# Kernel tuning notes

Hardware: AMD Instinct MI355X
Metric: run time of the kernel (lower is better)

The kernel has to match this reference:

```python
import jax, jax.numpy as jnp
import numpy as np

# Static 4-level feature pyramid (H, W) per level; total tokens = 20197
SHAPES = [(100, 152), (50, 76), (25, 38), (13, 19)]
B, S, E, H, L, P, R = 4, 1024, 256, 8, 4, 20, 4
HD = E // H
OFFSET_SCALE = 4.0


def setup_inputs() -> dict:
    key = jax.random.key(0)
    ks = jax.random.split(key, 11)
    total = sum(h * w for h, w in SHAPES)
    s = 0.02
    return {
        "x": jax.random.normal(ks[0], (B, S, E), jnp.float32),
        "encoder_input": jax.random.normal(ks[1], (B, total, E), jnp.float32),
        "v_w": jax.random.normal(ks[2], (E, E), jnp.float32) * s,
        "out_w": jax.random.normal(ks[3], (E, E), jnp.float32) * s,
        "off_w": jax.random.normal(ks[4], (H * L * P * 2, E), jnp.float32) * s,
        "off_b": jax.random.normal(ks[5], (H * L * P * 2,), jnp.float32) * s,
        "attn_w": jax.random.normal(ks[6], (H * L * P, E), jnp.float32) * s,
        "attn_b": jax.random.normal(ks[7], (H * L * P,), jnp.float32) * s,
        "ref_w": jax.random.normal(ks[8], (H * R, E), jnp.float32) * s,
        "ref_b": jax.random.normal(ks[9], (H * R,), jnp.float32) * s,
        "def_refs": jax.random.uniform(ks[10], (R, 2), jnp.float32, 0.1, 0.9),
        "spatial_shapes": jnp.array(SHAPES, dtype=jnp.int32),
    }


def _grid_sample(img, gx, gy, Hh, Ww):
    """Bilinear grid_sample, padding_mode='zeros', align_corners=False.
    img: (N, C, Hh*Ww); gx, gy: (N, M) in [-1, 1]. Returns (N, C, M)."""
    x = ((gx + 1.0) * Ww - 1.0) * 0.5
    y = ((gy + 1.0) * Hh - 1.0) * 0.5
    x0 = jnp.floor(x)
    y0 = jnp.floor(y)
    wx = x - x0
    wy = y - y0
    x0i = x0.astype(jnp.int32)
    y0i = y0.astype(jnp.int32)
    N, C, _ = img.shape

    def gather(xi, yi):
        valid = (xi >= 0) & (xi < Ww) & (yi >= 0) & (yi < Hh)
        idx = jnp.clip(yi, 0, Hh - 1) * Ww + jnp.clip(xi, 0, Ww - 1)
        v = jnp.take_along_axis(
            img, jnp.broadcast_to(idx[:, None, :], (N, C, idx.shape[-1])), axis=2)
        return v * valid[:, None, :].astype(img.dtype)

    return (gather(x0i, y0i) * ((1 - wx) * (1 - wy))[:, None, :]
            + gather(x0i + 1, y0i) * (wx * (1 - wy))[:, None, :]
            + gather(x0i, y0i + 1) * ((1 - wx) * wy)[:, None, :]
            + gather(x0i + 1, y0i + 1) * (wx * wy)[:, None, :])


def reference(x, encoder_input, v_w, out_w, off_w, off_b, attn_w, attn_b,
              ref_w, ref_b, def_refs, spatial_shapes):
    b, s, _ = x.shape
    values = (encoder_input @ v_w.T).reshape(b, -1, H, HD)
    refs = jax.nn.sigmoid(def_refs)  # (R, 2), default reference points
    ref_mix = jax.nn.softmax((x @ ref_w.T + ref_b).reshape(b, s, H, R), axis=-1)
    anchors = jnp.einsum('bshr,rc->bshc', ref_mix, refs)  # (b, s, H, 2)
    offsets = (x @ off_w.T + off_b).reshape(b, s, H, L, P, 2)
    attn = jax.nn.softmax((x @ attn_w.T + attn_b).reshape(b, s, H, L * P),
                          axis=-1).reshape(b, s, H, L, P)

    out = jnp.zeros((b, s, H, HD), x.dtype)
    start = 0
    for lvl, (hh, ww) in enumerate(SHAPES):  # static per-level loop (L=4)
        img = values[:, start:start + hh * ww]  # (b, hh*ww, H, HD)
        start += hh * ww
        img = img.transpose(0, 2, 3, 1).reshape(b * H, HD, hh * ww)
        norm = jnp.array([max(ww, 1), max(hh, 1)], x.dtype)
        locs = anchors[:, :, :, None, :] + jnp.tanh(offsets[:, :, :, lvl]) * (OFFSET_SCALE / norm)
        grid = jnp.clip(locs, 0.0, 1.0) * 2.0 - 1.0  # (b, s, H, P, 2)
        grid = grid.transpose(0, 2, 1, 3, 4).reshape(b * H, s * P, 2)
        sampled = _grid_sample(img, grid[..., 0], grid[..., 1], hh, ww)  # (b*H, HD, s*P)
        sampled = sampled.reshape(b, H, HD, s, P)
        out = out + jnp.einsum('bhcsp,bshp->bshc', sampled, attn[:, :, :, lvl])
    return out.reshape(b, s, E) @ out_w.T
```

## Files before the change

kernel.cpp:

```cpp
#include <hip/hip_runtime.h>
#include <hip/hip_bf16.h>
#include <math.h>

#define NH 8
#define HD 32
#define EDIM 256
#define NL 4
#define NP 20
#define NR 4
#define SEQ 1024
#define BATCH 4
#define TOTAL 20197
#define OFF_SCALE 4.0f

#define M_ENC (BATCH * TOTAL)
#define KDIM 256
#define LDSW 40

typedef short bf16x8 __attribute__((ext_vector_type(8)));
typedef float f32x4  __attribute__((ext_vector_type(4)));

__device__ __forceinline__ unsigned short f32_to_bf16_rne(float f) {
    unsigned u = __float_as_uint(f);
    return (unsigned short)((u + 0x7fffu + ((u >> 16) & 1u)) >> 16);
}

__global__ __launch_bounds__(256) void cast_f32_bf16_kernel(
    const float* __restrict__ src, unsigned short* __restrict__ dst,
    long n)
{
    long i = (long)blockIdx.x * blockDim.x + threadIdx.x;
    long stride = (long)gridDim.x * blockDim.x;
    for (long e = i * 8; e < n; e += stride * 8) {
        float4 a = *reinterpret_cast<const float4*>(src + e);
        float4 b = *reinterpret_cast<const float4*>(src + e + 4);
        float f[8] = {a.x, a.y, a.z, a.w, b.x, b.y, b.z, b.w};
        unsigned short o[8];
        #pragma unroll
        for (int j = 0; j < 8; ++j) o[j] = f32_to_bf16_rne(f[j]);
        *reinterpret_cast<uint4*>(dst + e) = *reinterpret_cast<const uint4*>(o);
    }
}

__global__ __launch_bounds__(256) void gemm_mfma_f32a_kernel(
    const float* __restrict__ A,
    const unsigned short* __restrict__ W,
    const float* __restrict__ bias,
    float* __restrict__ C,
    int M_real, int N)
{
    __shared__ __align__(16) unsigned short As[128 * LDSW];
    __shared__ __align__(16) unsigned short Ws[128 * LDSW];

    const int tid  = threadIdx.x;
    const int m0   = blockIdx.x * 128;
    const int n0   = blockIdx.y * 128;
    const int wave = tid >> 6;
    const int lane = tid & 63;
    const int wr   = wave >> 1;
    const int wc   = wave & 1;
    const int lrow = lane & 15;
    const int kg   = lane >> 4;

    f32x4 acc[4][4] = {};

    for (int k0 = 0; k0 < KDIM; k0 += 32) {
        #pragma unroll
        for (int p = 0; p < 4; ++p) {
            int s   = tid + p * 256;
            int row = s >> 3;
            int sl  = s & 7;
            int gm  = m0 + row;
            float4 v = make_float4(0.f, 0.f, 0.f, 0.f);
            if (gm < M_real)
                v = *reinterpret_cast<const float4*>(&A[(size_t)gm * KDIM + k0 + sl * 4]);
            unsigned short o[4] = {
                f32_to_bf16_rne(v.x), f32_to_bf16_rne(v.y),
                f32_to_bf16_rne(v.z), f32_to_bf16_rne(v.w)};
            *reinterpret_cast<uint2*>(&As[row * LDSW + sl * 4]) =
                *reinterpret_cast<const uint2*>(o);
        }
        #pragma unroll
        for (int it = 0; it < 2; ++it) {
            int s   = tid + it * 256;
            int row = s >> 2;
            int ks  = s & 3;
            uint4 vw = *reinterpret_cast<const uint4*>(
                W + (size_t)(n0 + row) * KDIM + k0 + ks * 8);
            *reinterpret_cast<uint4*>(&Ws[row * LDSW + ks * 8]) = vw;
        }
        __syncthreads();

        bf16x8 af[4], bfr[4];
        #pragma unroll
        for (int mi = 0; mi < 4; ++mi)
            af[mi] = *reinterpret_cast<const bf16x8*>(
                &As[(wr * 64 + mi * 16 + lrow) * LDSW + kg * 8]);
        #pragma unroll
        for (int nj = 0; nj < 4; ++nj)
            bfr[nj] = *reinterpret_cast<const bf16x8*>(
                &Ws[(wc * 64 + nj * 16 + lrow) * LDSW + kg * 8]);
        #pragma unroll
        for (int mi = 0; mi < 4; ++mi)
            #pragma unroll
            for (int nj = 0; nj < 4; ++nj)
                acc[mi][nj] = __builtin_amdgcn_mfma_f32_16x16x32_bf16(
                    af[mi], bfr[nj], acc[mi][nj], 0, 0, 0);
        __syncthreads();
    }

    #pragma unroll
    for (int mi = 0; mi < 4; ++mi) {
        #pragma unroll
        for (int nj = 0; nj < 4; ++nj) {
            int row_base = m0 + wr * 64 + mi * 16 + kg * 4;
            int col      = n0 + wc * 64 + nj * 16 + lrow;
            float bv = bias ? bias[col] : 0.f;
            #pragma unroll
            for (int r = 0; r < 4; ++r) {
                int row = row_base + r;
                if (row < M_real)
                    C[(size_t)row * N + col] = acc[mi][nj][r] + bv;
            }
        }
    }
}

__global__ __launch_bounds__(256) void gemm_atb_kernel(
    const float* __restrict__ A, const float* __restrict__ W,
    const float* __restrict__ bias, float* __restrict__ C,
    int M, int N, int K)
{
    __shared__ float As[16][64];
    __shared__ float Wt[16][64];

    const int tid = threadIdx.x;
    const int m0 = blockIdx.x * 64;
    const int n0 = blockIdx.y * 64;
    const int tx = tid & 15;
    const int ty = tid >> 4;
    const int lr = tid >> 2;
    const int lk = (tid & 3) << 2;

    const int am = m0 + lr;
    const int wn = n0 + lr;

    float acc[4][4] = {};

    for (int k0 = 0; k0 < K; k0 += 16) {
        float4 av = make_float4(0.f, 0.f, 0.f, 0.f);
        float4 wv = make_float4(0.f, 0.f, 0.f, 0.f);
        if (am < M) av = *reinterpret_cast<const float4*>(&A[(size_t)am * K + k0 + lk]);
        if (wn < N) wv = *reinterpret_cast<const float4*>(&W[(size_t)wn * K + k0 + lk]);
        As[lk + 0][lr] = av.x; As[lk + 1][lr] = av.y;
        As[lk + 2][lr] = av.z; As[lk + 3][lr] = av.w;
        Wt[lk + 0][lr] = wv.x; Wt[lk + 1][lr] = wv.y;
        Wt[lk + 2][lr] = wv.z; Wt[lk + 3][lr] = wv.w;
        __syncthreads();

        #pragma unroll
        for (int k = 0; k < 16; ++k) {
            float a[4], b[4];
            #pragma unroll
            for (int i = 0; i < 4; ++i) a[i] = As[k][ty * 4 + i];
            #pragma unroll
            for (int j = 0; j < 4; ++j) b[j] = Wt[k][tx * 4 + j];
            #pragma unroll
            for (int i = 0; i < 4; ++i)
                #pragma unroll
                for (int j = 0; j < 4; ++j)
                    acc[i][j] += a[i] * b[j];
        }
        __syncthreads();
    }

    #pragma unroll
    for (int i = 0; i < 4; ++i) {
        int m = m0 + ty * 4 + i;
        if (m >= M) continue;
        #pragma unroll
        for (int j = 0; j < 4; ++j) {
            int n = n0 + tx * 4 + j;
            if (n >= N) continue;
            float v = acc[i][j];
            if (bias) v += bias[n];
            C[(size_t)m * N + n] = v;
        }
    }
}

__global__ __launch_bounds__(256) void deform_sample_kernel(
    const float* __restrict__ values,
    const float* __restrict__ proj_off,
    const float* __restrict__ proj_attn,
    const float* __restrict__ proj_ref,
    const float* __restrict__ def_refs,
    float* __restrict__ out)
{
    const int row = blockIdx.x;
    const int b   = row >> 10;
    const int tid = threadIdx.x;

    __shared__ float  attn_s[NH * NL * NP];
    __shared__ float  anchors[NH][2];
    __shared__ unsigned int sidx[NH * NL * NP][2];
    __shared__ float4 wcor[NH * NL * NP];

    if (tid >= 96) {
        int i = tid - 96;
        reinterpret_cast<float4*>(attn_s)[i] =
            reinterpret_cast<const float4*>(proj_attn + (size_t)row * 640)[i];
    } else if (tid < NH) {
        const int h = tid;
        float rv[NR];
        float rmax = -1e30f;
        #pragma unroll
        for (int r = 0; r < NR; ++r) {
            rv[r] = proj_ref[(size_t)row * (NH * NR) + h * NR + r];
            rmax = fmaxf(rmax, rv[r]);
        }
        float rsum = 0.f;
        #pragma unroll
        for (int r = 0; r < NR; ++r) { rv[r] = __expf(rv[r] - rmax); rsum += rv[r]; }
        float ax = 0.f, ay = 0.f;
        #pragma unroll
        for (int r = 0; r < NR; ++r) {
            float pr = rv[r] / rsum;
            float sx = 1.f / (1.f + __expf(-def_refs[r * 2 + 0]));
            float sy = 1.f / (1.f + __expf(-def_refs[r * 2 + 1]));
            ax += pr * sx; ay += pr * sy;
        }
        anchors[h][0] = ax; anchors[h][1] = ay;
    }
    __syncthreads();

    {
        const int g = tid >> 5;
        const int l = tid & 31;
        float v0 = attn_s[g * 80 + l];
        float v1 = attn_s[g * 80 + 32 + l];
        float v2 = (l < 16) ? attn_s[g * 80 + 64 + l] : -1e30f;
        float m = fmaxf(fmaxf(v0, v1), v2);
        #pragma unroll
        for (int d = 16; d >= 1; d >>= 1) m = fmaxf(m, __shfl_xor(m, d, 64));
        float e0 = __expf(v0 - m), e1 = __expf(v1 - m);
        float e2 = (l < 16) ? __expf(v2 - m) : 0.f;
        float s = e0 + e1 + e2;
        #pragma unroll
        for (int d = 16; d >= 1; d >>= 1) s += __shfl_xor(s, d, 64);
        float inv = 1.f / s;
        __syncthreads();
        attn_s[g * 80 + l]      = e0 * inv;
        attn_s[g * 80 + 32 + l] = e1 * inv;
        if (l < 16) attn_s[g * 80 + 64 + l] = e2 * inv;
    }
    __syncthreads();

    const int lhh[NL] = {100, 50, 25, 13};
    const int lww[NL] = {152, 76, 38, 19};
    const int lst[NL] = {0, 15200, 19000, 19950};

    for (int e = tid; e < NH * NL * NP; e += 256) {
        int h = e / 80;
        int rem = e - h * 80;
        int l = rem / 20;
        const float2 o = *reinterpret_cast<const float2*>(
            proj_off + (size_t)row * 1280 + e * 2);
        float offx = tanhf(o.x);
        float offy = tanhf(o.y);
        int ww = lww[l], hh = lhh[l];
        float locx = fminf(fmaxf(anchors[h][0] + offx * (OFF_SCALE / (float)ww), 0.f), 1.f);
        float locy = fminf(fmaxf(anchors[h][1] + offy * (OFF_SCALE / (float)hh), 0.f), 1.f);
        float xx = locx * (float)ww - 0.5f;
        float yy = locy * (float)hh - 0.5f;
        float x0f = floorf(xx), y0f = floorf(yy);
        int x0 = (int)x0f, y0 = (int)y0f;
        float wx = xx - x0f, wy = yy - y0f;
        float wa = attn_s[e];

        float bx0 = (x0 >= 0)      ? 1.f : 0.f;
        float bx1 = (x0 < ww - 1)  ? 1.f : 0.f;
        float by0 = (y0 >= 0)      ? 1.f : 0.f;
        float by1 = (y0 < hh - 1)  ? 1.f : 0.f;
        int xc0 = max(x0, 0), xc1 = min(x0 + 1, ww - 1);
        int yc0 = max(y0, 0), yc1 = min(y0 + 1, hh - 1);
        unsigned int i00 = (unsigned int)(lst[l] + yc0 * ww + xc0);
        unsigned int i10 = (unsigned int)(lst[l] + yc0 * ww + xc1);
        unsigned int i01 = (unsigned int)(lst[l] + yc1 * ww + xc0);
        unsigned int i11 = (unsigned int)(lst[l] + yc1 * ww + xc1);

        float4 w;
        w.x = wa * (1.f - wx) * (1.f - wy) * bx0 * by0;
        w.y = wa * wx * (1.f - wy) * bx1 * by0;
        w.z = wa * (1.f - wx) * wy * bx0 * by1;
        w.w = wa * wx * wy * bx1 * by1;

        sidx[e][0] = i00 | (i10 << 16);
        sidx[e][1] = i01 | (i11 << 16);
        wcor[e] = w;
    }
    __syncthreads();

    const int h = tid >> 5;
    const int c = tid & 31;
    const float* vb = values + (size_t)b * TOTAL * 256 + h * 32 + c;
    float acc = 0.f;
    #pragma unroll 4
    for (int i = 0; i < 80; ++i) {
        int e = h * 80 + i;
        unsigned int p0 = sidx[e][0];
        unsigned int p1 = sidx[e][1];
        float4 w = wcor[e];
        float v00 = vb[(size_t)(p0 & 0xffffu) * 256];
        float v10 = vb[(size_t)(p0 >> 16) * 256];
        float v01 = vb[(size_t)(p1 & 0xffffu) * 256];
        float v11 = vb[(size_t)(p1 >> 16) * 256];
        acc += w.x * v00 + w.y * v10 + w.z * v01 + w.w * v11;
    }
    out[(size_t)row * 256 + h * 32 + c] = acc;
}

extern "C" void kernel_launch(void* const* d_in, const int* in_sizes, int n_in,
                              void* d_out, int out_size, void* d_ws, size_t ws_size,
                              hipStream_t stream)
{
    const float* x        = (const float*)d_in[0];
    const float* enc      = (const float*)d_in[1];
    const float* v_w      = (const float*)d_in[2];
    const float* out_w    = (const float*)d_in[3];
    const float* off_w    = (const float*)d_in[4];
    const float* off_b    = (const float*)d_in[5];
    const float* attn_w   = (const float*)d_in[6];
    const float* attn_b   = (const float*)d_in[7];
    const float* ref_w    = (const float*)d_in[8];
    const float* ref_b    = (const float*)d_in[9];
    const float* def_refs = (const float*)d_in[10];
    float* out = (float*)d_out;

    const int M_Q    = BATCH * SEQ;
    const int N_OFF  = NH * NL * NP * 2;
    const int N_ATTN = NH * NL * NP;
    const int N_REF  = NH * NR;

    float* ws = (float*)d_ws;
    float* values    = ws;
    float* proj_off  = values    + (size_t)M_ENC * EDIM;
    float* proj_attn = proj_off  + (size_t)M_Q * N_OFF;
    float* proj_ref  = proj_attn + (size_t)M_Q * N_ATTN;
    float* attn_out  = proj_ref  + (size_t)M_Q * N_REF;
    unsigned short* vw_bf16    = (unsigned short*)(attn_out + (size_t)M_Q * EDIM);
    unsigned short* offw_bf16  = vw_bf16   + (size_t)EDIM * KDIM;
    unsigned short* attnw_bf16 = offw_bf16 + (size_t)N_OFF * KDIM;

    dim3 blk(256);

    cast_f32_bf16_kernel<<<dim3(32), blk, 0, stream>>>(v_w, vw_bf16, (long)EDIM * KDIM);
    cast_f32_bf16_kernel<<<dim3(160), blk, 0, stream>>>(off_w, offw_bf16, (long)N_OFF * KDIM);
    cast_f32_bf16_kernel<<<dim3(80), blk, 0, stream>>>(attn_w, attnw_bf16, (long)N_ATTN * KDIM);

    gemm_mfma_f32a_kernel<<<dim3((M_ENC + 127) / 128, EDIM / 128), blk, 0, stream>>>(
        enc, vw_bf16, nullptr, values, M_ENC, EDIM);

    gemm_mfma_f32a_kernel<<<dim3(M_Q / 128, N_OFF / 128), blk, 0, stream>>>(
        x, offw_bf16, off_b, proj_off, M_Q, N_OFF);
    gemm_mfma_f32a_kernel<<<dim3(M_Q / 128, N_ATTN / 128), blk, 0, stream>>>(
        x, attnw_bf16, attn_b, proj_attn, M_Q, N_ATTN);
    gemm_atb_kernel<<<dim3(M_Q / 64, 1), blk, 0, stream>>>(
        x, ref_w, ref_b, proj_ref, M_Q, N_REF, EDIM);

    deform_sample_kernel<<<dim3(M_Q), blk, 0, stream>>>(
        values, proj_off, proj_attn, proj_ref, def_refs, attn_out);

    gemm_atb_kernel<<<dim3(M_Q / 64, EDIM / 64), blk, 0, stream>>>(
        attn_out, out_w, nullptr, out, M_Q, EDIM, EDIM);
}
```

Measured before the change: 334.6 us.

## Double-buffer MFMA GEMM, fuse ref projection into sampler, merge weight casts

The bf16 MFMA GEMM now double-buffers its LDS tiles, prefetching the next K tile into registers while computing the current one, which removes one barrier per iteration. The ref-weight projection is computed inside the deform sampling kernel, dropping a separate launch and its intermediate buffer. The three weight-cast kernels are merged into a single launch. Sample indices are stored pre-scaled as four 32-bit words read with one vector load, replacing 16-bit packing. In exchange, LDS and register use in the GEMM roughly double, and 32 threads per sampler block now do a serial 256-element dot product.

```diff
diff --git a/kernel.cpp b/kernel.cpp
--- a/kernel.cpp
+++ b/kernel.cpp
@@ -25,20 +25,27 @@
     return (unsigned short)((u + 0x7fffu + ((u >> 16) & 1u)) >> 16);
 }
 
-__global__ __launch_bounds__(256) void cast_f32_bf16_kernel(
-    const float* __restrict__ src, unsigned short* __restrict__ dst,
-    long n)
+__global__ __launch_bounds__(256) void cast3_kernel(
+    const float* __restrict__ s0, unsigned short* __restrict__ d0, long n0,
+    const float* __restrict__ s1, unsigned short* __restrict__ d1, long n1,
+    const float* __restrict__ s2, unsigned short* __restrict__ d2, long n2)
 {
-    long i = (long)blockIdx.x * blockDim.x + threadIdx.x;
+    long c0 = n0 >> 3, c1 = n1 >> 3, c2 = n2 >> 3;
+    long total = c0 + c1 + c2;
+    long gid = (long)blockIdx.x * blockDim.x + threadIdx.x;
     long stride = (long)gridDim.x * blockDim.x;
-    for (long e = i * 8; e < n; e += stride * 8) {
-        float4 a = *reinterpret_cast<const float4*>(src + e);
-        float4 b = *reinterpret_cast<const float4*>(src + e + 4);
+    for (long i = gid; i < total; i += stride) {
+        const float* s; unsigned short* d; long e;
+        if (i < c0)            { s = s0; d = d0; e = i * 8; }
+        else if (i < c0 + c1)  { s = s1; d = d1; e = (i - c0) * 8; }
+        else                   { s = s2; d = d2; e = (i - c0 - c1) * 8; }
+        float4 a = *reinterpret_cast<const float4*>(s + e);
+        float4 b = *reinterpret_cast<const float4*>(s + e + 4);
         float f[8] = {a.x, a.y, a.z, a.w, b.x, b.y, b.z, b.w};
         unsigned short o[8];
         #pragma unroll
         for (int j = 0; j < 8; ++j) o[j] = f32_to_bf16_rne(f[j]);
-        *reinterpret_cast<uint4*>(dst + e) = *reinterpret_cast<const uint4*>(o);
+        *reinterpret_cast<uint4*>(d + e) = *reinterpret_cast<const uint4*>(o);
     }
 }
 
@@ -49,8 +56,8 @@
     float* __restrict__ C,
     int M_real, int N)
 {
-    __shared__ __align__(16) unsigned short As[128 * LDSW];
-    __shared__ __align__(16) unsigned short Ws[128 * LDSW];
+    __shared__ __align__(16) unsigned short As[2][128 * LDSW];
+    __shared__ __align__(16) unsigned short Ws[2][128 * LDSW];
 
     const int tid  = threadIdx.x;
     const int m0   = blockIdx.x * 128;
@@ -62,51 +69,74 @@
     const int lrow = lane & 15;
     const int kg   = lane >> 4;
 
-    f32x4 acc[4][4] = {};
-
-    for (int k0 = 0; k0 < KDIM; k0 += 32) {
+    const int arow = tid >> 3;
+    const int asl  = tid & 7;
+    const int wrow = tid >> 2;
+    const int wks  = tid & 3;
+
+    f32x4  acc[4][4] = {};
+    float4 areg[4];
+    uint4  wreg[2];
+
+    auto LOADT = [&](int t) {
+        const int k0 = t * 32;
         #pragma unroll
         for (int p = 0; p < 4; ++p) {
-            int s   = tid + p * 256;
-            int row = s >> 3;
-            int sl  = s & 7;
-            int gm  = m0 + row;
+            int gm = m0 + arow + 32 * p;
             float4 v = make_float4(0.f, 0.f, 0.f, 0.f);
             if (gm < M_real)
-                v = *reinterpret_cast<const float4*>(&A[(size_t)gm * KDIM + k0 + sl * 4]);
+                v = *reinterpret_cast<const float4*>(
+                    &A[(size_t)gm * KDIM + k0 + asl * 4]);
+            areg[p] = v;
+        }
+        #pragma unroll
+        for (int it = 0; it < 2; ++it)
+            wreg[it] = *reinterpret_cast<const uint4*>(
+                &W[(size_t)(n0 + wrow + 64 * it) * KDIM + k0 + wks * 8]);
+    };
+    auto STORE = [&](int b) {
+        #pragma unroll
+        for (int p = 0; p < 4; ++p) {
             unsigned short o[4] = {
-                f32_to_bf16_rne(v.x), f32_to_bf16_rne(v.y),
-                f32_to_bf16_rne(v.z), f32_to_bf16_rne(v.w)};
-            *reinterpret_cast<uint2*>(&As[row * LDSW + sl * 4]) =
+                f32_to_bf16_rne(areg[p].x), f32_to_bf16_rne(areg[p].y),
+                f32_to_bf16_rne(areg[p].z), f32_to_bf16_rne(areg[p].w)};
+            *reinterpret_cast<uint2*>(&As[b][(arow + 32 * p) * LDSW + asl * 4]) =
                 *reinterpret_cast<const uint2*>(o);
         }
         #pragma unroll
-        for (int it = 0; it < 2; ++it) {
-            int s   = tid + it * 256;
-            int row = s >> 2;
-            int ks  = s & 3;
-            uint4 vw = *reinterpret_cast<const uint4*>(
-                W + (size_t)(n0 + row) * KDIM + k0 + ks * 8);
-            *reinterpret_cast<uint4*>(&Ws[row * LDSW + ks * 8]) = vw;
-        }
-        __syncthreads();
-
+        for (int it = 0; it < 2; ++it)
+            *reinterpret_cast<uint4*>(&Ws[b][(wrow + 64 * it) * LDSW + wks * 8]) =
+                wreg[it];
+    };
+    auto COMPUTE = [&](int b) {
         bf16x8 af[4], bfr[4];
         #pragma unroll
         for (int mi = 0; mi < 4; ++mi)
             af[mi] = *reinterpret_cast<const bf16x8*>(
-                &As[(wr * 64 + mi * 16 + lrow) * LDSW + kg * 8]);
+                &As[b][(wr * 64 + mi * 16 + lrow) * LDSW + kg * 8]);
         #pragma unroll
         for (int nj = 0; nj < 4; ++nj)
             bfr[nj] = *reinterpret_cast<const bf16x8*>(
-                &Ws[(wc * 64 + nj * 16 + lrow) * LDSW + kg * 8]);
+                &Ws[b][(wc * 64 + nj * 16 + lrow) * LDSW + kg * 8]);
         #pragma unroll
         for (int mi = 0; mi < 4; ++mi)
             #pragma unroll
             for (int nj = 0; nj < 4; ++nj)
                 acc[mi][nj] = __builtin_amdgcn_mfma_f32_16x16x32_bf16(
                     af[mi], bfr[nj], acc[mi][nj], 0, 0, 0);
-        __syncthreads();
+    };
+
+    LOADT(0);
+    STORE(0);
+    __syncthreads();
+    #pragma unroll
+    for (int t = 0; t < 8; ++t) {
+        if (t < 7) LOADT(t + 1);
+        COMPUTE(t & 1);
+        if (t < 7) {
+            STORE((t + 1) & 1);
+            __syncthreads();
+        }
     }
 
     #pragma unroll
@@ -191,9 +221,11 @@
 
 __global__ __launch_bounds__(256) void deform_sample_kernel(
     const float* __restrict__ values,
+    const float* __restrict__ x,
+    const float* __restrict__ ref_w,
+    const float* __restrict__ ref_b,
     const float* __restrict__ proj_off,
     const float* __restrict__ proj_attn,
-    const float* __restrict__ proj_ref,
     const float* __restrict__ def_refs,
     float* __restrict__ out)
 {
@@ -203,20 +235,35 @@
 
     __shared__ float  attn_s[NH * NL * NP];
     __shared__ float  anchors[NH][2];
-    __shared__ unsigned int sidx[NH * NL * NP][2];
+    __shared__ float  refv[NH * NR];
+    __shared__ __align__(16) unsigned int sidx[NH * NL * NP][4];
     __shared__ float4 wcor[NH * NL * NP];
 
     if (tid >= 96) {
         int i = tid - 96;
         reinterpret_cast<float4*>(attn_s)[i] =
             reinterpret_cast<const float4*>(proj_attn + (size_t)row * 640)[i];
-    } else if (tid < NH) {
+    } else if (tid < 32) {
+        float dot = ref_b[tid];
+        const float* xr = x + (size_t)row * 256;
+        const float* wr = ref_w + (size_t)tid * 256;
+        for (int k = 0; k < 256; k += 4) {
+            float4 xv = *reinterpret_cast<const float4*>(xr + k);
+            float4 wv = *reinterpret_cast<const float4*>(wr + k);
+            dot += xv.x * wv.x; dot += xv.y * wv.y;
+            dot += xv.z * wv.z; dot += xv.w * wv.w;
+        }
+        refv[tid] = dot;
+    }
+    __syncthreads();
+
+    if (tid < NH) {
         const int h = tid;
         float rv[NR];
         float rmax = -1e30f;
         #pragma unroll
         for (int r = 0; r < NR; ++r) {
-            rv[r] = proj_ref[(size_t)row * (NH * NR) + h * NR + r];
+            rv[r] = refv[h * NR + r];
             rmax = fmaxf(rmax, rv[r]);
         }
         float rsum = 0.f;
@@ -232,8 +279,6 @@
         }
         anchors[h][0] = ax; anchors[h][1] = ay;
     }
-    __syncthreads();
-
     {
         const int g = tid >> 5;
         const int l = tid & 31;
@@ -284,19 +329,16 @@
         float by1 = (y0 < hh - 1)  ? 1.f : 0.f;
         int xc0 = max(x0, 0), xc1 = min(x0 + 1, ww - 1);
         int yc0 = max(y0, 0), yc1 = min(y0 + 1, hh - 1);
-        unsigned int i00 = (unsigned int)(lst[l] + yc0 * ww + xc0);
-        unsigned int i10 = (unsigned int)(lst[l] + yc0 * ww + xc1);
-        unsigned int i01 = (unsigned int)(lst[l] + yc1 * ww + xc0);
-        unsigned int i11 = (unsigned int)(lst[l] + yc1 * ww + xc1);
+        sidx[e][0] = (unsigned int)(lst[l] + yc0 * ww + xc0) << 8;
+        sidx[e][1] = (unsigned int)(lst[l] + yc0 * ww + xc1) << 8;
+        sidx[e][2] = (unsigned int)(lst[l] + yc1 * ww + xc0) << 8;
+        sidx[e][3] = (unsigned int)(lst[l] + yc1 * ww + xc1) << 8;
 
         float4 w;
         w.x = wa * (1.f - wx) * (1.f - wy) * bx0 * by0;
         w.y = wa * wx * (1.f - wy) * bx1 * by0;
         w.z = wa * (1.f - wx) * wy * bx0 * by1;
         w.w = wa * wx * wy * bx1 * by1;
-
-        sidx[e][0] = i00 | (i10 << 16);
-        sidx[e][1] = i01 | (i11 << 16);
         wcor[e] = w;
     }
     __syncthreads();
@@ -308,14 +350,12 @@
     #pragma unroll 4
     for (int i = 0; i < 80; ++i) {
         int e = h * 80 + i;
-        unsigned int p0 = sidx[e][0];
-        unsigned int p1 = sidx[e][1];
+        uint4 pi = *reinterpret_cast<const uint4*>(&sidx[e][0]);
         float4 w = wcor[e];
-        float v00 = vb[(size_t)(p0 & 0xffffu) * 256];
-        float v10 = vb[(size_t)(p0 >> 16) * 256];
-        float v01 = vb[(size_t)(p1 & 0xffffu) * 256];
-        float v11 = vb[(size_t)(p1 >> 16) * 256];
-        acc += w.x * v00 + w.y * v10 + w.z * v01 + w.w * v11;
+        acc += w.x * vb[pi.x];
+        acc += w.y * vb[pi.y];
+        acc += w.z * vb[pi.z];
+        acc += w.w * vb[pi.w];
     }
     out[(size_t)row * 256 + h * 32 + c] = acc;
 }
@@ -340,23 +380,22 @@
     const int M_Q    = BATCH * SEQ;
     const int N_OFF  = NH * NL * NP * 2;
     const int N_ATTN = NH * NL * NP;
-    const int N_REF  = NH * NR;
 
     float* ws = (float*)d_ws;
     float* values    = ws;
     float* proj_off  = values    + (size_t)M_ENC * EDIM;
     float* proj_attn = proj_off  + (size_t)M_Q * N_OFF;
-    float* proj_ref  = proj_attn + (size_t)M_Q * N_ATTN;
-    float* attn_out  = proj_ref  + (size_t)M_Q * N_REF;
+    float* attn_out  = proj_attn + (size_t)M_Q * N_ATTN;
     unsigned short* vw_bf16    = (unsigned short*)(attn_out + (size_t)M_Q * EDIM);
     unsigned short* offw_bf16  = vw_bf16   + (size_t)EDIM * KDIM;
     unsigned short* attnw_bf16 = offw_bf16 + (size_t)N_OFF * KDIM;
 
     dim3 blk(256);
 
-    cast_f32_bf16_kernel<<<dim3(32), blk, 0, stream>>>(v_w, vw_bf16, (long)EDIM * KDIM);
-    cast_f32_bf16_kernel<<<dim3(160), blk, 0, stream>>>(off_w, offw_bf16, (long)N_OFF * KDIM);
-    cast_f32_bf16_kernel<<<dim3(80), blk, 0, stream>>>(attn_w, attnw_bf16, (long)N_ATTN * KDIM);
+    cast3_kernel<<<dim3(272), blk, 0, stream>>>(
+        v_w, vw_bf16, (long)EDIM * KDIM,
+        off_w, offw_bf16, (long)N_OFF * KDIM,
+        attn_w, attnw_bf16, (long)N_ATTN * KDIM);
 
     gemm_mfma_f32a_kernel<<<dim3((M_ENC + 127) / 128, EDIM / 128), blk, 0, stream>>>(
         enc, vw_bf16, nullptr, values, M_ENC, EDIM);
@@ -365,11 +404,9 @@
         x, offw_bf16, off_b, proj_off, M_Q, N_OFF);
     gemm_mfma_f32a_kernel<<<dim3(M_Q / 128, N_ATTN / 128), blk, 0, stream>>>(
         x, attnw_bf16, attn_b, proj_attn, M_Q, N_ATTN);
-    gemm_atb_kernel<<<dim3(M_Q / 64, 1), blk, 0, stream>>>(
-        x, ref_w, ref_b, proj_ref, M_Q, N_REF, EDIM);
 
     deform_sample_kernel<<<dim3(M_Q), blk, 0, stream>>>(
-        values, proj_off, proj_attn, proj_ref, def_refs, attn_out);
+        values, x, ref_w, ref_b, proj_off, proj_attn, def_refs, attn_out);
 
     gemm_atb_kernel<<<dim3(M_Q / 64, EDIM / 64), blk, 0, stream>>>(
         attn_out, out_w, nullptr, out, M_Q, EDIM, EDIM);
```

Result: no change. 329.6 us (-1.5%).
